# Kernel tuning notes

Measured on AMD Instinct MI355X. Metric: run time of the kernel, lower is better.

The kernel has to match this reference:

```python
import jax, jax.numpy as jnp
import numpy as np
import math

B, L, D = 4, 4096, 768          # batch, seq_len (== l_max), d_model
ORDER, EMB_DIM = 16, 3          # hyena_filter_order, hyena_emb_dim
W_MOD = 1.0                     # hyena_w_mod
FAST, SLOW, TARGET = 0.3, 1.5, 1e-2  # ExponentialModulation defaults


def setup_inputs() -> dict:
    key = jax.random.key(0)
    ks = jax.random.split(key, 16)
    n = lambda i, shape, s: jax.random.normal(ks[i], shape, dtype=jnp.float32) * s
    # PositionalEmbedding buffer/param z, deterministic Hyena init (seq_len = l_max = L)
    t = np.linspace(0.0, 1.0, L)[None, :, None]
    bands = (EMB_DIM - 1) // 2
    t_re = np.linspace(0, L - 1, L)[None, :, None]
    w = 2 * math.pi * t_re / L
    f = np.linspace(1e-4, bands - 1, bands)[None, None]
    zc = np.exp(-1j * f * w)
    z = np.concatenate([t, zc.real, zc.imag], axis=-1).astype(np.float32)  # (1, L, 3)
    return {
        "u": jax.random.normal(ks[0], (B, L, D), dtype=jnp.float32),
        "w_in": n(1, (3 * D, D), 0.02),
        "b_in": jnp.zeros((3 * D,), jnp.float32),
        "w_out": n(2, (D, D), 0.02),
        "b_out": jnp.zeros((D,), jnp.float32),
        "conv_w": n(3, (3 * D, 1, 3), 0.3),   # depthwise Conv1d weight (O, I/groups=1, K)
        "conv_b": jnp.zeros((3 * D,), jnp.float32),
        "z": jnp.asarray(z),
        "fw1": n(4, (ORDER, EMB_DIM), 0.3),
        "fb1": n(5, (ORDER,), 0.3),
        "fw2": n(6, (ORDER, ORDER), 0.3),
        "fb2": n(7, (ORDER,), 0.3),
        "fw3": n(8, (ORDER, ORDER), 0.3),
        "fb3": n(9, (ORDER,), 0.3),
        "fw4": n(10, (D, ORDER), 0.3),
        "freq": jnp.full((1, ORDER), 10.0, jnp.float32),  # shared Sin freq, init w*ones
        "filter_bias": jax.random.normal(ks[11], (D,), dtype=jnp.float32),
    }


def _hyena_filter(z, fw1, fb1, fw2, fb2, fw3, fb3, fw4, freq, Lq):
    # implicit MLP with SHARED Sin activation (same freq param at all 3 activations)
    sin = lambda h: jnp.sin(W_MOD * freq * h)
    h = sin(z @ fw1.T + fb1)
    h = sin(h @ fw2.T + fb2)
    h = sin(h @ fw3.T + fb3)
    h = h @ fw4.T                                     # (1, L, D)
    # ExponentialModulation
    max_d = math.log(TARGET) / FAST
    min_d = math.log(TARGET) / SLOW
    deltas = jnp.linspace(min_d, max_d, D)[None, None]  # (1, 1, D)
    t = jnp.linspace(0.0, 1.0, Lq)[None, :, None]       # (1, L, 1)
    h = h * jnp.exp(-t * jnp.abs(deltas))
    return h[0].T                                      # (D, L)


def _fftconv(v, k, bias):
    # causal FFT long conv: fft_size = 2L, torch norm='forward' conventions
    Lq = v.shape[-1]
    nfft = 2 * Lq
    k_f = jnp.fft.rfft(k, n=nfft) / nfft               # (D, nfft//2+1)
    v_f = jnp.fft.rfft(v, n=nfft)                      # (B, D, nfft//2+1)
    y = jnp.fft.irfft(v_f * k_f, n=nfft, norm="forward")[..., :Lq]
    return y + v * bias[None, :, None]


def reference(u, w_in, b_in, w_out, b_out, conv_w, conv_b, z,
              fw1, fb1, fw2, fb2, fw3, fb3, fw4, freq, filter_bias):
    Bq, Lq, Dq = u.shape
    x = u @ w_in.T + b_in                              # (B, L, 3D)
    x = x.transpose(0, 2, 1)                           # (B, 3D, L)
    # depthwise short conv, kernel 3, padding 2, sliced to [:L]
    xc = jax.lax.conv_general_dilated(
        x, conv_w, window_strides=(1,), padding=[(2, 2)],
        feature_group_count=3 * Dq,
        dimension_numbers=("NCH", "OIH", "NCH"))[..., :Lq]
    xc = xc + conv_b[None, :, None]
    x1, x2, v = jnp.split(xc, 3, axis=1)               # each (B, D, L)
    v = v * x1                                         # pre-gate
    k = _hyena_filter(z[:, :Lq], fw1, fb1, fw2, fb2, fw3, fb3, fw4, freq, Lq)
    y = _fftconv(v, k, filter_bias) * x2               # long conv + post-gate
    y = y.transpose(0, 2, 1) @ w_out.T + b_out         # (B, L, D)
    return y
```

## Files before the change

kernel.cpp:

```cpp
#include <hip/hip_runtime.h>

#define BB 4
#define LL 4096
#define DD 768
#define TD 2304
#define NFFT 8192
#define PI2 6.283185307179586f

__device__ __forceinline__ unsigned short f2b(float f) {
    unsigned u = __float_as_uint(f);
    unsigned r = (u + 0x7fffu + ((u >> 16) & 1u)) >> 16;
    return (unsigned short)r;
}
__device__ __forceinline__ float b2f(unsigned short h) {
    return __uint_as_float((unsigned)h << 16);
}

typedef __bf16 bf16x8 __attribute__((ext_vector_type(8)));
typedef float  f32x4  __attribute__((ext_vector_type(4)));

constexpr float TWC[16] = {
    1.f, 0.98078528f, 0.92387953f, 0.83146961f,
    0.70710678f, 0.55557023f, 0.38268343f, 0.19509032f,
    0.f, -0.19509032f, -0.38268343f, -0.55557023f,
    -0.70710678f, -0.83146961f, -0.92387953f, -0.98078528f};
constexpr float TWS[16] = {
    0.f, 0.19509032f, 0.38268343f, 0.55557023f,
    0.70710678f, 0.83146961f, 0.92387953f, 0.98078528f,
    1.f, 0.98078528f, 0.92387953f, 0.83146961f,
    0.70710678f, 0.55557023f, 0.38268343f, 0.19509032f};

template<int LOGN, bool INV>
__device__ __forceinline__ void reg_fft(float2* R) {
    constexpr int N = 1 << LOGN;
#pragma unroll
    for (int i = 0; i < N; ++i) {
        int j = 0;
#pragma unroll
        for (int b = 0; b < LOGN; ++b) if (i & (1 << b)) j |= (1 << (LOGN - 1 - b));
        if (j > i) { float2 tt = R[i]; R[i] = R[j]; R[j] = tt; }
    }
#pragma unroll
    for (int s = 1; s <= LOGN; ++s) {
        const int hm = 1 << (s - 1);
        const int tsh = 5 - s;
#pragma unroll
        for (int g = 0; g < N; g += (hm << 1)) {
#pragma unroll
            for (int j2 = 0; j2 < hm; ++j2) {
                const float wr = TWC[j2 << tsh];
                const float wi = INV ? TWS[j2 << tsh] : -TWS[j2 << tsh];
                float2 u = R[g + j2];
                float2 v = R[g + j2 + hm];
                float vr = v.x * wr - v.y * wi;
                float vi = v.x * wi + v.y * wr;
                R[g + j2]      = make_float2(u.x + vr, u.y + vi);
                R[g + j2 + hm] = make_float2(u.x - vr, u.y - vi);
            }
        }
    }
}

template<int NN>
__device__ __forceinline__ void ramp_mul(float2* R, float ang) {
    float s0, c0; __sincosf(ang, &s0, &c0);
    float wr = c0, wi = s0;
#pragma unroll
    for (int k = 1; k < NN; ++k) {
        float xr = R[k].x, xi = R[k].y;
        R[k] = make_float2(xr * wr - xi * wi, xr * wi + xi * wr);
        float nr = wr * c0 - wi * s0;
        float ni = wr * s0 + wi * c0;
        wr = nr; wi = ni;
    }
}

#define A1(t, k2) ((k2) * 288 + (t) + ((t) >> 3))
#define A2(k2, p, r) ((k2) * 272 + (r) * 17 + (p))
#define FFT_LDS 9216

__device__ __forceinline__ void eng_fwd(float2* buf, float2* R, int t) {
    reg_fft<5, false>(R);
    ramp_mul<32>(R, -PI2 * (float)t / 8192.0f);
    __syncthreads();
#pragma unroll
    for (int k2 = 0; k2 < 32; ++k2) buf[A1(t, k2)] = R[k2];
    __syncthreads();
    const int p = t & 15, c2 = (t >> 4) << 1;
#pragma unroll
    for (int q = 0; q < 16; ++q) {
        R[q]      = buf[A1(p + 16 * q, c2)];
        R[16 + q] = buf[A1(p + 16 * q, c2 + 1)];
    }
    reg_fft<4, false>(R);
    reg_fft<4, false>(R + 16);
    float a2 = -PI2 * (float)p / 256.0f;
    ramp_mul<16>(R, a2);
    ramp_mul<16>(R + 16, a2);
    __syncthreads();
#pragma unroll
    for (int r = 0; r < 16; ++r) {
        buf[A2(c2, p, r)]     = R[r];
        buf[A2(c2 + 1, p, r)] = R[16 + r];
    }
    __syncthreads();
    const int rr = p;
#pragma unroll
    for (int pp = 0; pp < 16; ++pp) {
        R[pp]      = buf[A2(c2, pp, rr)];
        R[16 + pp] = buf[A2(c2 + 1, pp, rr)];
    }
    reg_fft<4, false>(R);
    reg_fft<4, false>(R + 16);
}

__device__ __forceinline__ void eng_inv(float2* buf, float2* R, int t) {
    const int p = t & 15, c2 = (t >> 4) << 1, rr = p;
    reg_fft<4, true>(R);
    reg_fft<4, true>(R + 16);
    __syncthreads();
#pragma unroll
    for (int pp = 0; pp < 16; ++pp) {
        buf[A2(c2, pp, rr)]     = R[pp];
        buf[A2(c2 + 1, pp, rr)] = R[16 + pp];
    }
    __syncthreads();
#pragma unroll
    for (int r = 0; r < 16; ++r) {
        R[r]      = buf[A2(c2, p, r)];
        R[16 + r] = buf[A2(c2 + 1, p, r)];
    }
    float a2 = PI2 * (float)p / 256.0f;
    ramp_mul<16>(R, a2);
    ramp_mul<16>(R + 16, a2);
    reg_fft<4, true>(R);
    reg_fft<4, true>(R + 16);
    __syncthreads();
#pragma unroll
    for (int q = 0; q < 16; ++q) {
        buf[A1(p + 16 * q, c2)]     = R[q];
        buf[A1(p + 16 * q, c2 + 1)] = R[16 + q];
    }
    __syncthreads();
#pragma unroll
    for (int k2 = 0; k2 < 32; ++k2) R[k2] = buf[A1(t, k2)];
    ramp_mul<32>(R, PI2 * (float)t / 8192.0f);
    reg_fft<5, true>(R);
}

__global__ __launch_bounds__(256) void k_cast_pair(
        const float* __restrict__ srcA, unsigned long long nA4,
        const float* __restrict__ srcB, unsigned long long nB4,
        unsigned short* __restrict__ dstA, unsigned short* __restrict__ dstB) {
    unsigned long long i = (unsigned long long)blockIdx.x * 256 + threadIdx.x;
    const float* s; unsigned short* d;
    if (i < nA4)            { s = srcA + i * 4;         d = dstA + i * 4; }
    else if (i < nA4 + nB4) { unsigned long long j = i - nA4; s = srcB + j * 4; d = dstB + j * 4; }
    else return;
    float4 v = *(const float4*)s;
    unsigned long long p = (unsigned long long)f2b(v.x)
                         | ((unsigned long long)f2b(v.y) << 16)
                         | ((unsigned long long)f2b(v.z) << 32)
                         | ((unsigned long long)f2b(v.w) << 48);
    *(unsigned long long*)d = p;
}

#define GEMM_BODY(EPILOGUE)                                                     \
    __shared__ unsigned char AsB[16384];                                        \
    __shared__ unsigned char BsB[16384];                                        \
    const int tid  = threadIdx.x;                                               \
    const int lane = tid & 63;                                                  \
    const int w    = tid >> 6;                                                  \
    const int wr   = w >> 1, wc = w & 1;                                        \
    const int m0 = blockIdx.y * 128, n0 = blockIdx.x * 128;                     \
    f32x4 acc[4][4] = {};                                                       \
    const int srow = lane >> 3;                    \
    const int sslot = (lane & 7) ^ srow;          \
    for (int k0 = 0; k0 < K; k0 += 64) {                                        \
        _Pragma("unroll")                                                       \
        for (int c = 0; c < 4; ++c) {                                           \
            int chunk = w * 4 + c;                                              \
            int row = chunk * 8 + srow;                                         \
            const char* ga = (const char*)A  + (((size_t)(m0 + row) * K + k0) * 2) + sslot * 16; \
            __builtin_amdgcn_global_load_lds(                                   \
                (const __attribute__((address_space(1))) void*)ga,              \
                (__attribute__((address_space(3))) void*)(AsB + chunk * 1024), 16, 0, 0); \
            const char* gb = (const char*)Bw + (((size_t)(n0 + row) * K + k0) * 2) + sslot * 16; \
            __builtin_amdgcn_global_load_lds(                                   \
                (const __attribute__((address_space(1))) void*)gb,              \
                (__attribute__((address_space(3))) void*)(BsB + chunk * 1024), 16, 0, 0); \
        }                                                                       \
        __syncthreads();                                                        \
        const int quad = lane >> 4;                                             \
        const int rsel = lane & 15;                                             \
        _Pragma("unroll")                                                       \
        for (int kk = 0; kk < 2; ++kk) {                                        \
            bf16x8 af[4], bfr[4];                                               \
            _Pragma("unroll")                                                   \
            for (int i = 0; i < 4; ++i) {                                       \
                int rowA = wr * 64 + i * 16 + rsel;                             \
                int slotA = (kk * 4 + quad) ^ (rsel & 7);                       \
                af[i]  = *(const bf16x8*)(AsB + rowA * 128 + slotA * 16);       \
                int rowB = wc * 64 + i * 16 + rsel;                             \
                bfr[i] = *(const bf16x8*)(BsB + rowB * 128 + slotA * 16);       \
            }                                                                   \
            _Pragma("unroll")                                                   \
            for (int i = 0; i < 4; ++i)                                         \
                _Pragma("unroll")                                               \
                for (int j = 0; j < 4; ++j)                                     \
                    acc[i][j] = __builtin_amdgcn_mfma_f32_16x16x32_bf16(af[i], bfr[j], acc[i][j], 0, 0, 0); \
        }                                                                       \
        __syncthreads();                                                        \
    }                                                                           \
    const int cq = lane >> 4;                                                   \
    const int cn = lane & 15;                                                   \
    _Pragma("unroll")                                                           \
    for (int j = 0; j < 4; ++j) {                                               \
        int col = n0 + wc * 64 + j * 16 + cn;                                   \
        float bv = bias[col];                                                   \
        _Pragma("unroll")                                                       \
        for (int i = 0; i < 4; ++i) {                                           \
            int rbase = m0 + wr * 64 + i * 16 + cq * 4;                         \
            _Pragma("unroll")                                                   \
            for (int r = 0; r < 4; ++r)                                         \
                EPILOGUE;                                                       \
        }                                                                       \
    }

__global__ __launch_bounds__(256) void k_gemm_mfma_b16(
        const unsigned short* __restrict__ A, const unsigned short* __restrict__ Bw,
        const float* __restrict__ bias, unsigned short* __restrict__ C,
        int N, int K) {
    GEMM_BODY(C[(size_t)(rbase + r) * N + col] = f2b(acc[i][j][r] + bv))
}

__global__ __launch_bounds__(256) void k_gemm_mfma(
        const unsigned short* __restrict__ A, const unsigned short* __restrict__ Bw,
        const float* __restrict__ bias, float* __restrict__ C,
        int N, int K) {
    GEMM_BODY(C[(size_t)(rbase + r) * N + col] = acc[i][j][r] + bv)
}

__global__ __launch_bounds__(256) void k_shortconv(
        const unsigned short* __restrict__ x, const float* __restrict__ conv_w,
        const float* __restrict__ conv_b,
        unsigned short* __restrict__ vbuf, unsigned short* __restrict__ x2buf) {
    __shared__ float xs[3][32][66];
    const int l0 = blockIdx.x * 64;
    const int d0 = blockIdx.y * 32;
    const int b  = blockIdx.z;
    const int tid = threadIdx.x;
    for (int idx = tid; idx < 3 * 66 * 16; idx += 256) {
        int g  = idx / (66 * 16);
        int r  = idx % (66 * 16);
        int ll = r >> 4;
        int dd2 = (r & 15) * 2;
        int gl = l0 - 2 + ll;
        float v0 = 0.f, v1 = 0.f;
        if (gl >= 0) {
            unsigned int pk = *(const unsigned int*)&x[((size_t)(b * LL + gl)) * TD + g * DD + d0 + dd2];
            v0 = b2f((unsigned short)(pk & 0xffffu));
            v1 = b2f((unsigned short)(pk >> 16));
        }
        xs[g][dd2][ll] = v0;
        xs[g][dd2 + 1][ll] = v1;
    }
    __syncthreads();
    const int tl  = tid & 63;
    const int tdq = tid >> 6;
    for (int dd = tdq; dd < 32; dd += 4) {
        int c0 = d0 + dd;
        const float* w0 = conv_w + (size_t)c0 * 3;
        const float* w1 = conv_w + (size_t)(DD + c0) * 3;
        const float* w2 = conv_w + (size_t)(2 * DD + c0) * 3;
        float x1v = w0[0]*xs[0][dd][tl] + w0[1]*xs[0][dd][tl+1] + w0[2]*xs[0][dd][tl+2] + conv_b[c0];
        float x2v = w1[0]*xs[1][dd][tl] + w1[1]*xs[1][dd][tl+1] + w1[2]*xs[1][dd][tl+2] + conv_b[DD + c0];
        float vv  = w2[0]*xs[2][dd][tl] + w2[1]*xs[2][dd][tl+1] + w2[2]*xs[2][dd][tl+2] + conv_b[2*DD + c0];
        size_t o = ((size_t)(b * DD + c0)) * LL + l0 + tl;
        vbuf[o]  = f2b(vv * x1v);
        x2buf[o] = f2b(x2v);
    }
}

__global__ __launch_bounds__(256) void k_filter_mlp(
        const float* __restrict__ z,
        const float* __restrict__ fw1, const float* __restrict__ fb1,
        const float* __restrict__ fw2, const float* __restrict__ fb2,
        const float* __restrict__ fw3, const float* __restrict__ fb3,
        const float* __restrict__ freq, float* __restrict__ h3g) {
    int l = blockIdx.x * 256 + threadIdx.x;
    float z0 = z[l*3+0], z1 = z[l*3+1], z2 = z[l*3+2];
    float h1[16], h2[16];
#pragma unroll
    for (int j = 0; j < 16; ++j) {
        float a = z0*fw1[j*3+0] + z1*fw1[j*3+1] + z2*fw1[j*3+2] + fb1[j];
        h1[j] = sinf(freq[j] * a);
    }
#pragma unroll
    for (int j = 0; j < 16; ++j) {
        float a = fb2[j];
#pragma unroll
        for (int i = 0; i < 16; ++i) a += h1[i] * fw2[j*16+i];
        h2[j] = sinf(freq[j] * a);
    }
#pragma unroll
    for (int j = 0; j < 16; ++j) {
        float a = fb3[j];
#pragma unroll
        for (int i = 0; i < 16; ++i) a += h2[i] * fw3[j*16+i];
        h3g[j * LL + l] = sinf(freq[j] * a);
    }
}

__global__ __launch_bounds__(256) void k_filter_fft(
        const float* __restrict__ h3g, const float* __restrict__ fw4,
        const float* __restrict__ fbias, float2* __restrict__ kf) {
    __shared__ float2 buf[FFT_LDS];
    const int d = blockIdx.x, t = threadIdx.x;
    float w4[16];
#pragma unroll
    for (int i = 0; i < 16; ++i) w4[i] = fw4[d * 16 + i];
    const float min_d = 3.070113457325394f;
    const float max_d = 15.35056728662697f;
    const float ad = min_d + (max_d - min_d) * ((float)d / 767.0f);
    float2 R[32];
#pragma unroll
    for (int j = 0; j < 16; ++j) {
        int l = t + 256 * j;
        float acc = 0.f;
#pragma unroll
        for (int i = 0; i < 16; ++i) acc += h3g[i * LL + l] * w4[i];
        acc *= __expf(-((float)l / 4095.0f) * ad);
        R[j] = make_float2(acc, 0.f);
        R[16 + j] = make_float2(0.f, 0.f);
    }
    eng_fwd(buf, R, t);
    const float fb = fbias[d];
    const float inv_n = 1.0f / (float)NFFT;
    float2* kd = kf + (size_t)d * NFFT;
#pragma unroll
    for (int i = 0; i < 32; ++i)
        kd[i * 256 + t] = make_float2((R[i].x + fb) * inv_n, R[i].y * inv_n);
}

__global__ __launch_bounds__(256) void k_fftconv3(
        const unsigned short* __restrict__ vbuf, const float2* __restrict__ kf,
        unsigned short* __restrict__ x2y) {
    __shared__ float2 buf[FFT_LDS];
    const int bp = blockIdx.x;
    const int d = bp % DD;
    const int bpair = bp / DD;
    const size_t row1 = (size_t)(bpair * 2) * DD + d;
    const size_t row2 = row1 + DD;
    const unsigned short* v1 = vbuf + row1 * LL;
    const unsigned short* v2 = vbuf + row2 * LL;
    const int t = threadIdx.x;
    float2 R[32];
#pragma unroll
    for (int j = 0; j < 16; ++j) {
        int idx = t + 256 * j;
        R[j] = make_float2(b2f(v1[idx]), b2f(v2[idx]));
        R[16 + j] = make_float2(0.f, 0.f);
    }
    eng_fwd(buf, R, t);
    const float2* kd = kf + (size_t)d * NFFT;
#pragma unroll
    for (int i = 0; i < 32; ++i) {
        float2 w = kd[i * 256 + t];
        float2 zv = R[i];
        R[i] = make_float2(zv.x * w.x - zv.y * w.y, zv.x * w.y + zv.y * w.x);
    }
    eng_inv(buf, R, t);
    unsigned short* o1 = x2y + row1 * LL;
    unsigned short* o2 = x2y + row2 * LL;
#pragma unroll
    for (int j = 0; j < 16; ++j) {
        int idx = t + 256 * j;
        o1[idx] = f2b(R[j].x * b2f(o1[idx]));
        o2[idx] = f2b(R[j].y * b2f(o2[idx]));
    }
}

__global__ __launch_bounds__(256) void k_transpose_cast(
        const unsigned short* __restrict__ yg, unsigned short* __restrict__ ygT) {
    __shared__ float t[64][65];
    const int b = blockIdx.z;
    const int d0 = blockIdx.y * 64;
    const int l0 = blockIdx.x * 64;
    for (int idx = threadIdx.x; idx < 4096; idx += 256) {
        int r = idx >> 6, c = idx & 63;
        t[r][c] = b2f(yg[((size_t)(b * DD + d0 + r)) * LL + l0 + c]);
    }
    __syncthreads();
    for (int idx = threadIdx.x; idx < 2048; idx += 256) {
        int r = idx >> 5, c = (idx & 31) * 2;
        unsigned int p = (unsigned int)f2b(t[c][r]) | ((unsigned int)f2b(t[c+1][r]) << 16);
        *(unsigned int*)&ygT[((size_t)(b * LL + l0 + r)) * DD + d0 + c] = p;
    }
}

extern "C" void kernel_launch(void* const* d_in, const int* in_sizes, int n_in,
                              void* d_out, int out_size, void* d_ws, size_t ws_size,
                              hipStream_t stream) {
    const float* u      = (const float*)d_in[0];
    const float* w_in   = (const float*)d_in[1];
    const float* b_in   = (const float*)d_in[2];
    const float* w_out  = (const float*)d_in[3];
    const float* b_out  = (const float*)d_in[4];
    const float* conv_w = (const float*)d_in[5];
    const float* conv_b = (const float*)d_in[6];
    const float* z      = (const float*)d_in[7];
    const float* fw1    = (const float*)d_in[8];
    const float* fb1    = (const float*)d_in[9];
    const float* fw2    = (const float*)d_in[10];
    const float* fb2    = (const float*)d_in[11];
    const float* fw3    = (const float*)d_in[12];
    const float* fb3    = (const float*)d_in[13];
    const float* fw4    = (const float*)d_in[14];
    const float* freq   = (const float*)d_in[15];
    const float* fbias  = (const float*)d_in[16];

    char* ws = (char*)d_ws;
    unsigned short* x_bf     = (unsigned short*)(ws);
    float2* kf               = (float2*)(ws);
    float*  h3g              = (float*)(ws + 50331648);
    unsigned short* w_out_bf = (unsigned short*)(ws + 50593792);
    unsigned short* ygT      = (unsigned short*)(ws + 63176704);
    unsigned short* vbuf     = (unsigned short*)(ws + 150994944);
    unsigned short* x2y      = (unsigned short*)(ws + 176160768);
    unsigned short* u_bf     = (unsigned short*)(ws + 201326592);
    unsigned short* w_in_bf  = (unsigned short*)(ws + 226492416);

    k_cast_pair<<<(3145728 + 442368 + 255) / 256, 256, 0, stream>>>(
        u, 3145728ULL, w_in, 442368ULL, u_bf, w_in_bf);
    k_gemm_mfma_b16<<<dim3(TD/128, (BB*LL)/128), 256, 0, stream>>>(u_bf, w_in_bf, b_in, x_bf, TD, DD);
    k_shortconv<<<dim3(LL/64, DD/32, BB), 256, 0, stream>>>(x_bf, conv_w, conv_b, vbuf, x2y);
    k_filter_mlp<<<LL/256, 256, 0, stream>>>(z, fw1, fb1, fw2, fb2, fw3, fb3, freq, h3g);
    k_filter_fft<<<DD, 256, 0, stream>>>(h3g, fw4, fbias, kf);
    k_cast_pair<<<(147456 + 255) / 256, 256, 0, stream>>>(
        w_out, 147456ULL, (const float*)0, 0ULL, w_out_bf, (unsigned short*)0);
    k_fftconv3<<<(BB/2)*DD, 256, 0, stream>>>(vbuf, kf, x2y);
    k_transpose_cast<<<dim3(LL/64, DD/64, BB), 256, 0, stream>>>(x2y, ygT);
    k_gemm_mfma<<<dim3(DD/128, (BB*LL)/128), 256, 0, stream>>>(ygT, w_out_bf, b_out, (float*)d_out, DD, DD);
}
```

Baseline: 422.3 us.

## Write first GEMM output transposed and simplify short conv to row-wise loads

The input projection GEMM now stores its bf16 output transposed as (B, 3D, L), writing packed 4-element runs along L with a hardware pack-convert instruction. The short-conv kernel then reads each channel's row contiguously, with one block per (batch, channel) and 16 positions per thread, which removes the shared-memory transpose stage. Both GEMMs also remap block IDs across groups of 8, an XCD-style swizzle meant to improve L2 locality. The transposed GEMM stores are only 8 bytes each and strided by L per column, so write coalescing could suffer.

```diff
diff --git a/kernel.cpp b/kernel.cpp
--- a/kernel.cpp
+++ b/kernel.cpp
@@ -14,6 +14,11 @@
 }
 __device__ __forceinline__ float b2f(unsigned short h) {
     return __uint_as_float((unsigned)h << 16);
+}
+__device__ __forceinline__ unsigned cvt_pk_bf16(float lo, float hi) {
+    unsigned r;
+    asm("v_cvt_pk_bf16_f32 %0, %1, %2" : "=v"(r) : "v"(lo), "v"(hi));
+    return r;
 }
 
 typedef __bf16 bf16x8 __attribute__((ext_vector_type(8)));
@@ -165,14 +170,18 @@
     *(unsigned long long*)d = p;
 }
 
-#define GEMM_BODY(EPILOGUE)                                                     \
+#define GEMM_CORE                                                               \
     __shared__ unsigned char AsB[16384];                                        \
     __shared__ unsigned char BsB[16384];                                        \
     const int tid  = threadIdx.x;                                               \
     const int lane = tid & 63;                                                  \
     const int w    = tid >> 6;                                                  \
     const int wr   = w >> 1, wc = w & 1;                                        \
-    const int m0 = blockIdx.y * 128, n0 = blockIdx.x * 128;                     \
+    const int nbx  = (int)gridDim.x;                                            \
+    int bid = (int)blockIdx.y * nbx + (int)blockIdx.x;                          \
+    { const int cpx = (nbx * (int)gridDim.y) >> 3;                              \
+      bid = (bid & 7) * cpx + (bid >> 3); }                                     \
+    const int m0 = (bid / nbx) * 128, n0 = (bid % nbx) * 128;                   \
     f32x4 acc[4][4] = {};                                                       \
     const int srow = lane >> 3;                    \
     const int sslot = (lane & 7) ^ srow;          \
@@ -211,75 +220,106 @@
                     acc[i][j] = __builtin_amdgcn_mfma_f32_16x16x32_bf16(af[i], bfr[j], acc[i][j], 0, 0, 0); \
         }                                                                       \
         __syncthreads();                                                        \
-    }                                                                           \
-    const int cq = lane >> 4;                                                   \
-    const int cn = lane & 15;                                                   \
-    _Pragma("unroll")                                                           \
-    for (int j = 0; j < 4; ++j) {                                               \
-        int col = n0 + wc * 64 + j * 16 + cn;                                   \
-        float bv = bias[col];                                                   \
-        _Pragma("unroll")                                                       \
-        for (int i = 0; i < 4; ++i) {                                           \
-            int rbase = m0 + wr * 64 + i * 16 + cq * 4;                         \
-            _Pragma("unroll")                                                   \
-            for (int r = 0; r < 4; ++r)                                         \
-                EPILOGUE;                                                       \
-        }                                                                       \
-    }
-
-__global__ __launch_bounds__(256) void k_gemm_mfma_b16(
+    }
+
+__global__ __launch_bounds__(256) void k_gemm1_xt(
         const unsigned short* __restrict__ A, const unsigned short* __restrict__ Bw,
-        const float* __restrict__ bias, unsigned short* __restrict__ C,
-        int N, int K) {
-    GEMM_BODY(C[(size_t)(rbase + r) * N + col] = f2b(acc[i][j][r] + bv))
+        const float* __restrict__ bias, unsigned short* __restrict__ xT,
+        int K) {
+    GEMM_CORE
+    const int cq = lane >> 4;
+    const int cn = lane & 15;
+    const int b  = m0 >> 12;
+    const int lb = (m0 & 4095) + wr * 64 + cq * 4;
+#pragma unroll
+    for (int j = 0; j < 4; ++j) {
+        int col = n0 + wc * 64 + j * 16 + cn;
+        float bv = bias[col];
+        unsigned short* cp = xT + ((size_t)b * TD + col) * LL + lb;
+#pragma unroll
+        for (int i = 0; i < 4; ++i) {
+            uint2 p;
+            p.x = cvt_pk_bf16(acc[i][j][0] + bv, acc[i][j][1] + bv);
+            p.y = cvt_pk_bf16(acc[i][j][2] + bv, acc[i][j][3] + bv);
+            *(uint2*)(cp + i * 16) = p;
+        }
+    }
 }
 
 __global__ __launch_bounds__(256) void k_gemm_mfma(
         const unsigned short* __restrict__ A, const unsigned short* __restrict__ Bw,
         const float* __restrict__ bias, float* __restrict__ C,
         int N, int K) {
-    GEMM_BODY(C[(size_t)(rbase + r) * N + col] = acc[i][j][r] + bv)
-}
-
-__global__ __launch_bounds__(256) void k_shortconv(
-        const unsigned short* __restrict__ x, const float* __restrict__ conv_w,
-        const float* __restrict__ conv_b,
+    GEMM_CORE
+    const int cq = lane >> 4;
+    const int cn = lane & 15;
+#pragma unroll
+    for (int j = 0; j < 4; ++j) {
+        int col = n0 + wc * 64 + j * 16 + cn;
+        float bv = bias[col];
+#pragma unroll
+        for (int i = 0; i < 4; ++i) {
+            int rbase = m0 + wr * 64 + i * 16 + cq * 4;
+#pragma unroll
+            for (int r = 0; r < 4; ++r)
+                C[(size_t)(rbase + r) * N + col] = acc[i][j][r] + bv;
+        }
+    }
+}
+
+__device__ __forceinline__ void ld_row18(const unsigned short* __restrict__ r,
+                                         int l0, float* a) {
+    unsigned ql = 0;
+    if (l0 >= 2) ql = *(const unsigned*)(r + l0 - 2);
+    a[0] = b2f((unsigned short)(ql & 0xffffu));
+    a[1] = b2f((unsigned short)(ql >> 16));
+    uint4 q0 = *(const uint4*)(r + l0);
+    uint4 q1 = *(const uint4*)(r + l0 + 8);
+    unsigned qq[8] = {q0.x, q0.y, q0.z, q0.w, q1.x, q1.y, q1.z, q1.w};
+#pragma unroll
+    for (int k2 = 0; k2 < 8; ++k2) {
+        a[2 + 2 * k2] = b2f((unsigned short)(qq[k2] & 0xffffu));
+        a[3 + 2 * k2] = b2f((unsigned short)(qq[k2] >> 16));
+    }
+}
+
+__global__ __launch_bounds__(256) void k_shortconv_t(
+        const unsigned short* __restrict__ xT,
+        const float* __restrict__ conv_w, const float* __restrict__ conv_b,
         unsigned short* __restrict__ vbuf, unsigned short* __restrict__ x2buf) {
-    __shared__ float xs[3][32][66];
-    const int l0 = blockIdx.x * 64;
-    const int d0 = blockIdx.y * 32;
-    const int b  = blockIdx.z;
-    const int tid = threadIdx.x;
-    for (int idx = tid; idx < 3 * 66 * 16; idx += 256) {
-        int g  = idx / (66 * 16);
-        int r  = idx % (66 * 16);
-        int ll = r >> 4;
-        int dd2 = (r & 15) * 2;
-        int gl = l0 - 2 + ll;
-        float v0 = 0.f, v1 = 0.f;
-        if (gl >= 0) {
-            unsigned int pk = *(const unsigned int*)&x[((size_t)(b * LL + gl)) * TD + g * DD + d0 + dd2];
-            v0 = b2f((unsigned short)(pk & 0xffffu));
-            v1 = b2f((unsigned short)(pk >> 16));
-        }
-        xs[g][dd2][ll] = v0;
-        xs[g][dd2 + 1][ll] = v1;
-    }
-    __syncthreads();
-    const int tl  = tid & 63;
-    const int tdq = tid >> 6;
-    for (int dd = tdq; dd < 32; dd += 4) {
-        int c0 = d0 + dd;
-        const float* w0 = conv_w + (size_t)c0 * 3;
-        const float* w1 = conv_w + (size_t)(DD + c0) * 3;
-        const float* w2 = conv_w + (size_t)(2 * DD + c0) * 3;
-        float x1v = w0[0]*xs[0][dd][tl] + w0[1]*xs[0][dd][tl+1] + w0[2]*xs[0][dd][tl+2] + conv_b[c0];
-        float x2v = w1[0]*xs[1][dd][tl] + w1[1]*xs[1][dd][tl+1] + w1[2]*xs[1][dd][tl+2] + conv_b[DD + c0];
-        float vv  = w2[0]*xs[2][dd][tl] + w2[1]*xs[2][dd][tl+1] + w2[2]*xs[2][dd][tl+2] + conv_b[2*DD + c0];
-        size_t o = ((size_t)(b * DD + c0)) * LL + l0 + tl;
-        vbuf[o]  = f2b(vv * x1v);
-        x2buf[o] = f2b(x2v);
-    }
+    const int bd = blockIdx.x;
+    const int b  = bd / DD;
+    const int d  = bd - b * DD;
+    const int l0 = (int)threadIdx.x << 4;
+    const unsigned short* r1 = xT + ((size_t)b * TD + d) * LL;
+    const unsigned short* r2 = r1 + (size_t)DD * LL;
+    const unsigned short* r3 = r2 + (size_t)DD * LL;
+    const float w10 = conv_w[3*d],          w11 = conv_w[3*d+1],          w12 = conv_w[3*d+2];
+    const float w20 = conv_w[3*(DD+d)],     w21 = conv_w[3*(DD+d)+1],     w22 = conv_w[3*(DD+d)+2];
+    const float w30 = conv_w[3*(2*DD+d)],   w31 = conv_w[3*(2*DD+d)+1],   w32 = conv_w[3*(2*DD+d)+2];
+    const float c1 = conv_b[d], c2 = conv_b[DD + d], c3 = conv_b[2*DD + d];
+    float a1[18], a2[18], a3[18];
+    ld_row18(r1, l0, a1);
+    ld_row18(r2, l0, a2);
+    ld_row18(r3, l0, a3);
+    unsigned pv[8], px[8];
+#pragma unroll
+    for (int k2 = 0; k2 < 8; ++k2) {
+        float x1a = w10*a1[2*k2]   + w11*a1[2*k2+1] + w12*a1[2*k2+2] + c1;
+        float x1b = w10*a1[2*k2+1] + w11*a1[2*k2+2] + w12*a1[2*k2+3] + c1;
+        float x2a = w20*a2[2*k2]   + w21*a2[2*k2+1] + w22*a2[2*k2+2] + c2;
+        float x2b = w20*a2[2*k2+1] + w21*a2[2*k2+2] + w22*a2[2*k2+3] + c2;
+        float va  = w30*a3[2*k2]   + w31*a3[2*k2+1] + w32*a3[2*k2+2] + c3;
+        float vb  = w30*a3[2*k2+1] + w31*a3[2*k2+2] + w32*a3[2*k2+3] + c3;
+        pv[k2] = cvt_pk_bf16(va * x1a, vb * x1b);
+        px[k2] = cvt_pk_bf16(x2a, x2b);
+    }
+    unsigned short* ov = vbuf  + ((size_t)b * DD + d) * LL + l0;
+    unsigned short* ox = x2buf + ((size_t)b * DD + d) * LL + l0;
+    *(uint4*)(ov)     = make_uint4(pv[0], pv[1], pv[2], pv[3]);
+    *(uint4*)(ov + 8) = make_uint4(pv[4], pv[5], pv[6], pv[7]);
+    *(uint4*)(ox)     = make_uint4(px[0], px[1], px[2], px[3]);
+    *(uint4*)(ox + 8) = make_uint4(px[4], px[5], px[6], px[7]);
 }
 
 __global__ __launch_bounds__(256) void k_filter_mlp(
@@ -433,8 +473,8 @@
 
     k_cast_pair<<<(3145728 + 442368 + 255) / 256, 256, 0, stream>>>(
         u, 3145728ULL, w_in, 442368ULL, u_bf, w_in_bf);
-    k_gemm_mfma_b16<<<dim3(TD/128, (BB*LL)/128), 256, 0, stream>>>(u_bf, w_in_bf, b_in, x_bf, TD, DD);
-    k_shortconv<<<dim3(LL/64, DD/32, BB), 256, 0, stream>>>(x_bf, conv_w, conv_b, vbuf, x2y);
+    k_gemm1_xt<<<dim3(TD/128, (BB*LL)/128), 256, 0, stream>>>(u_bf, w_in_bf, b_in, x_bf, DD);
+    k_shortconv_t<<<BB*DD, 256, 0, stream>>>(x_bf, conv_w, conv_b, vbuf, x2y);
     k_filter_mlp<<<LL/256, 256, 0, stream>>>(z, fw1, fb1, fw2, fb2, fw3, fb3, freq, h3g);
     k_filter_fft<<<DD, 256, 0, stream>>>(h3g, fw4, fbias, kf);
     k_cast_pair<<<(147456 + 255) / 256, 256, 0, stream>>>(
```

Result: faster. 410.3 us (-2.9%).
